# Optimization experiments

Measured on AMD Instinct MI355X. Metric: run time of the kernel, lower is better.

The kernel has to match this reference:

```python
import jax, jax.numpy as jnp
import numpy as np

NUM_HEADS = 12
MASK_BIAS = -1000.0


def setup_inputs() -> dict:
    key = jax.random.key(0)
    k1, k2, k3, k4 = jax.random.split(key, 4)
    B, N, C = 2, 2048, 768
    x = jax.random.normal(k1, (B, N, C), dtype=jnp.float32)
    # key-padding mask: 1.0 = masked-out position (gets -1000 bias), 0.0 = visible
    mask = jax.random.randint(k2, (B, N), 0, 2).astype(jnp.float32)
    qkv_w = jax.random.normal(k3, (3 * C, C), dtype=jnp.float32) * (1.0 / np.sqrt(C))
    proj_w = jax.random.normal(k4, (C, C), dtype=jnp.float32) * (1.0 / np.sqrt(C))
    proj_b = jnp.zeros((C,), dtype=jnp.float32)
    return {"x": x, "mask": mask, "qkv_w": qkv_w, "proj_w": proj_w, "proj_b": proj_b}


def reference(x, mask, qkv_w, proj_w, proj_b):
    B, N, C = x.shape
    H = NUM_HEADS
    D = C // H
    scale = D ** (-0.5)
    # qkv: Linear without bias -> [B, N, 3C] -> [3, B, H, N, D]
    qkv = (x @ qkv_w.T).reshape(B, N, 3, H, D).transpose(2, 0, 3, 1, 4)
    q, k, v = qkv[0], qkv[1], qkv[2]
    # scores [B, H, N, N]
    attn = jnp.einsum("bhqd,bhkd->bhqk", q, k) * scale
    attn = attn + mask[:, None, None, :] * MASK_BIAS
    attn = jax.nn.softmax(attn, axis=-1)
    out = jnp.einsum("bhqk,bhkd->bhqd", attn, v)  # [B, H, N, D]
    out = out.transpose(0, 2, 1, 3).reshape(B, N, C)
    return out @ proj_w.T + proj_b
```

## Files before the change

### kernel.cpp

```cpp
#include <hip/hip_runtime.h>

typedef __bf16 bf16_t;
typedef __bf16 bf16x8 __attribute__((ext_vector_type(8)));
typedef float f32x4 __attribute__((ext_vector_type(4)));

#define NUM_B 2
#define NUM_H 12
#define SEQ_N 2048
#define DIM_C 768
#define HEAD_D 64
#define BH_CNT (NUM_B * NUM_H)
#define MTOK (NUM_B * SEQ_N)
#define QSCALE 0.1803368801111137f

#define AS1(p) ((const __attribute__((address_space(1))) void*)(p))
#define AS3(p) ((__attribute__((address_space(3))) void*)(p))

__global__ __launch_bounds__(256) void cvt_kernel(
    const float* __restrict__ s0, const float* __restrict__ s1,
    const float* __restrict__ s2, const float* __restrict__ msk,
    bf16_t* __restrict__ d0, bf16_t* __restrict__ d1, bf16_t* __restrict__ d2,
    bf16_t* __restrict__ dw, int nb0, int nb1, int nb2) {
  const int blk = blockIdx.x;
  const float* src;
  bf16_t* dst;
  size_t off;
  bool isw = false;
  if (blk < nb0) {
    src = s0; dst = d0; off = (size_t)blk * 2048;
  } else if (blk < nb0 + nb1) {
    src = s1; dst = d1; off = (size_t)(blk - nb0) * 2048;
  } else if (blk < nb0 + nb1 + nb2) {
    src = s2; dst = d2; off = (size_t)(blk - nb0 - nb1) * 2048;
  } else {
    src = msk; dst = dw; off = (size_t)(blk - nb0 - nb1 - nb2) * 2048;
    isw = true;
  }
  const size_t i = off + (size_t)threadIdx.x * 8;
  float4 f0 = *reinterpret_cast<const float4*>(&src[i]);
  float4 f1 = *reinterpret_cast<const float4*>(&src[i + 4]);
  if (isw) {
    f0 = {1.0f - f0.x, 1.0f - f0.y, 1.0f - f0.z, 1.0f - f0.w};
    f1 = {1.0f - f1.x, 1.0f - f1.y, 1.0f - f1.z, 1.0f - f1.w};
  }
  union { ushort4 u; bf16_t h[4]; } p0, p1;
  p0.h[0] = (bf16_t)f0.x; p0.h[1] = (bf16_t)f0.y;
  p0.h[2] = (bf16_t)f0.z; p0.h[3] = (bf16_t)f0.w;
  p1.h[0] = (bf16_t)f1.x; p1.h[1] = (bf16_t)f1.y;
  p1.h[2] = (bf16_t)f1.z; p1.h[3] = (bf16_t)f1.w;
  *reinterpret_cast<ushort4*>(&dst[i]) = p0.u;
  *reinterpret_cast<ushort4*>(&dst[i + 4]) = p1.u;
}

__global__ __launch_bounds__(256, 3) void gemm_qkv_kernel(
    const bf16_t* __restrict__ A, const bf16_t* __restrict__ W,
    const float* __restrict__ mask, bf16_t* __restrict__ out) {
  __shared__ __align__(16) bf16_t As[2][128 * 32];
  __shared__ __align__(16) bf16_t Bs[2][128 * 32];

  const int tid = threadIdx.x;
  const int wave = tid >> 6, lane = tid & 63;
  const int quad = lane >> 4, l16 = lane & 15;
  const int m0 = blockIdx.y * 128, n0 = blockIdx.x * 128;
  const int wm = (wave >> 1) * 64, wn = (wave & 1) * 64;
  const bool vmode = (n0 >= 2 * DIM_C);

  f32x4 acc[4][4] = {};

  const int srow = tid >> 2;
  const int scol = ((tid & 3) ^ ((tid >> 3) & 3)) * 8;
  const bf16_t* gA0 = A + (size_t)(m0 + srow) * DIM_C + scol;
  const bf16_t* gA1 = A + (size_t)(m0 + srow + 64) * DIM_C + scol;
  const bf16_t* gB0 = W + (size_t)(n0 + srow) * DIM_C + scol;
  const bf16_t* gB1 = W + (size_t)(n0 + srow + 64) * DIM_C + scol;
  const int lb = wave * 512;

  auto issue = [&](int buf, int k0) {
    __builtin_amdgcn_global_load_lds(AS1(gA0 + k0), AS3(&As[buf][lb]), 16, 0, 0);
    __builtin_amdgcn_global_load_lds(AS1(gA1 + k0), AS3(&As[buf][lb + 2048]), 16, 0, 0);
    __builtin_amdgcn_global_load_lds(AS1(gB0 + k0), AS3(&Bs[buf][lb]), 16, 0, 0);
    __builtin_amdgcn_global_load_lds(AS1(gB1 + k0), AS3(&Bs[buf][lb + 2048]), 16, 0, 0);
  };

  issue(0, 0);
  int cur = 0;
  const int sw = (l16 >> 1) & 3;
  for (int step = 0; step < DIM_C / 32; ++step) {
    __syncthreads();
    if (step + 1 < DIM_C / 32) issue(cur ^ 1, (step + 1) * 32);

    bf16x8 aF[4], bF[4];
#pragma unroll
    for (int mi = 0; mi < 4; ++mi)
      aF[mi] = *reinterpret_cast<const bf16x8*>(
          &As[cur][(wm + mi * 16 + l16) * 32 + ((quad ^ sw) * 8)]);
#pragma unroll
    for (int ni = 0; ni < 4; ++ni)
      bF[ni] = *reinterpret_cast<const bf16x8*>(
          &Bs[cur][(wn + ni * 16 + l16) * 32 + ((quad ^ sw) * 8)]);
    if (vmode) {
#pragma unroll
      for (int mi = 0; mi < 4; ++mi)
#pragma unroll
        for (int ni = 0; ni < 4; ++ni)
          acc[mi][ni] = __builtin_amdgcn_mfma_f32_16x16x32_bf16(
              bF[ni], aF[mi], acc[mi][ni], 0, 0, 0);
    } else {
#pragma unroll
      for (int mi = 0; mi < 4; ++mi)
#pragma unroll
        for (int ni = 0; ni < 4; ++ni)
          acc[mi][ni] = __builtin_amdgcn_mfma_f32_16x16x32_bf16(
              aF[mi], bF[ni], acc[mi][ni], 0, 0, 0);
    }
    cur ^= 1;
  }

  if (!vmode) {
#pragma unroll
    for (int mi = 0; mi < 4; ++mi) {
#pragma unroll
      for (int ni = 0; ni < 4; ++ni) {
        const int gmB = m0 + wm + mi * 16 + quad * 4;
        const int gn = n0 + wn + ni * 16 + l16;
        const int which = gn / DIM_C;
        const int rem = gn - which * DIM_C;
        const int h = rem >> 6, d = rem & 63;
        const float sc = (which == 0) ? QSCALE : 1.0f;
        const size_t base = (size_t)which * ((size_t)BH_CNT * SEQ_N * HEAD_D);
#pragma unroll
        for (int r = 0; r < 4; ++r) {
          const int gm = gmB + r;
          const int b = gm >> 11, tok = gm & 2047;
          out[base + (((size_t)(b * NUM_H + h) * SEQ_N + tok) * HEAD_D + d)] =
              (bf16_t)(acc[mi][ni][r] * sc);
        }
      }
    }
  } else {
    const size_t base = 2ull * BH_CNT * SEQ_N * HEAD_D;
#pragma unroll
    for (int mi = 0; mi < 4; ++mi) {
      const int tok = m0 + wm + mi * 16 + l16;
      const float wvf = 1.0f - mask[tok];
      const int b = tok >> 11, tokm = tok & 2047;
#pragma unroll
      for (int ni = 0; ni < 4; ++ni) {
#pragma unroll
        for (int r = 0; r < 4; ++r) {
          const int rowg = n0 - 2 * DIM_C + wn + ni * 16 + quad * 4 + r;
          const int h = rowg >> 6, d = rowg & 63;
          out[base + (((size_t)(b * NUM_H + h) * HEAD_D + d) * SEQ_N + tokm)] =
              (bf16_t)(acc[mi][ni][r] * wvf);
        }
      }
    }
  }
}

__global__ __launch_bounds__(256, 4) void gemm_proj_kernel(
    const bf16_t* __restrict__ A, const bf16_t* __restrict__ W,
    const float* __restrict__ bias, float* __restrict__ out) {
  __shared__ __align__(16) bf16_t As[2][64 * 32];
  __shared__ __align__(16) bf16_t Bs[2][64 * 32];

  const int tid = threadIdx.x;
  const int wave = tid >> 6, lane = tid & 63;
  const int quad = lane >> 4, l16 = lane & 15;
  const int m0 = blockIdx.y * 64, n0 = blockIdx.x * 64;
  const int wm = (wave >> 1) * 32, wn = (wave & 1) * 32;

  f32x4 acc[2][2] = {};

  const int srow = tid >> 2;
  const int scol = ((tid & 3) ^ ((tid >> 3) & 3)) * 8;
  const bf16_t* gA = A + (size_t)(m0 + srow) * DIM_C + scol;
  const bf16_t* gB = W + (size_t)(n0 + srow) * DIM_C + scol;
  const int lb = wave * 512;

  auto issue = [&](int buf, int k0) {
    __builtin_amdgcn_global_load_lds(AS1(gA + k0), AS3(&As[buf][lb]), 16, 0, 0);
    __builtin_amdgcn_global_load_lds(AS1(gB + k0), AS3(&Bs[buf][lb]), 16, 0, 0);
  };

  issue(0, 0);
  int cur = 0;
  const int sw = (l16 >> 1) & 3;
  for (int step = 0; step < DIM_C / 32; ++step) {
    __syncthreads();
    if (step + 1 < DIM_C / 32) issue(cur ^ 1, (step + 1) * 32);

    bf16x8 aF[2], bF[2];
#pragma unroll
    for (int mi = 0; mi < 2; ++mi)
      aF[mi] = *reinterpret_cast<const bf16x8*>(
          &As[cur][(wm + mi * 16 + l16) * 32 + ((quad ^ sw) * 8)]);
#pragma unroll
    for (int ni = 0; ni < 2; ++ni)
      bF[ni] = *reinterpret_cast<const bf16x8*>(
          &Bs[cur][(wn + ni * 16 + l16) * 32 + ((quad ^ sw) * 8)]);
#pragma unroll
    for (int mi = 0; mi < 2; ++mi)
#pragma unroll
      for (int ni = 0; ni < 2; ++ni)
        acc[mi][ni] = __builtin_amdgcn_mfma_f32_16x16x32_bf16(aF[mi], bF[ni],
                                                              acc[mi][ni], 0, 0, 0);
    cur ^= 1;
  }

#pragma unroll
  for (int mi = 0; mi < 2; ++mi) {
#pragma unroll
    for (int ni = 0; ni < 2; ++ni) {
      const int gmB = m0 + wm + mi * 16 + quad * 4;
      const int gn = n0 + wn + ni * 16 + l16;
      const float bv = bias[gn];
#pragma unroll
      for (int r = 0; r < 4; ++r)
        out[(size_t)(gmB + r) * DIM_C + gn] = acc[mi][ni][r] + bv;
    }
  }
}

__global__ __launch_bounds__(256, 4) void attn_kernel(
    const bf16_t* __restrict__ q, const bf16_t* __restrict__ k,
    const bf16_t* __restrict__ vt, const bf16_t* __restrict__ wv,
    bf16_t* __restrict__ ctx) {
  __shared__ __align__(16) bf16_t Ks[2][64 * 64];
  __shared__ __align__(16) bf16_t Vs[2][64 * 64];
  __shared__ __align__(16) bf16_t Ps[4][1024];

  const int tid = threadIdx.x;
  const int wave = tid >> 6, lane = tid & 63;
  const int quad = lane >> 4, l16 = lane & 15;
  const int bh = blockIdx.y;
  const int b = bh / NUM_H, h = bh - b * NUM_H;
  const int q0 = blockIdx.x * 64 + wave * 16;

  const bf16_t* qb = q + (size_t)bh * SEQ_N * HEAD_D;
  const bf16_t* kb = k + (size_t)bh * SEQ_N * HEAD_D;
  const bf16_t* vtb = vt + (size_t)bh * HEAD_D * SEQ_N;
  const bf16_t* wb = wv + (size_t)b * SEQ_N;

  bf16x8 qf[2];
#pragma unroll
  for (int ks = 0; ks < 2; ++ks)
    qf[ks] = *reinterpret_cast<const bf16x8*>(
        &qb[(size_t)(q0 + l16) * HEAD_D + ks * 32 + quad * 8]);

  f32x4 acc[4] = {};
  f32x4 acc_l = {};

  const int srow = tid >> 3;
  const int scol = ((tid & 7) ^ ((tid >> 3) & 7)) * 8;
  const bf16_t* gK0 = kb + (size_t)srow * HEAD_D + scol;
  const bf16_t* gK1 = kb + (size_t)(srow + 32) * HEAD_D + scol;
  const bf16_t* gV0 = vtb + (size_t)srow * SEQ_N + scol;
  const bf16_t* gV1 = vtb + (size_t)(srow + 32) * SEQ_N + scol;
  const int lb = wave * 512;

  auto issueKV = [&](int buf, int key0) {
    __builtin_amdgcn_global_load_lds(AS1(gK0 + (size_t)key0 * HEAD_D),
                                     AS3(&Ks[buf][lb]), 16, 0, 0);
    __builtin_amdgcn_global_load_lds(AS1(gK1 + (size_t)key0 * HEAD_D),
                                     AS3(&Ks[buf][lb + 2048]), 16, 0, 0);
    __builtin_amdgcn_global_load_lds(AS1(gV0 + key0), AS3(&Vs[buf][lb]), 16, 0, 0);
    __builtin_amdgcn_global_load_lds(AS1(gV1 + key0), AS3(&Vs[buf][lb + 2048]),
                                     16, 0, 0);
  };

  issueKV(0, 0);
  int cur = 0;
  const int swz = l16 & 7;
  const int psbase = wave * 1024 + l16 * 64;
  for (int key0 = 0; key0 < SEQ_N; key0 += 64) {
    __syncthreads();
    if (key0 + 64 < SEQ_N) issueKV(cur ^ 1, key0 + 64);

    f32x4 s[4];
#pragma unroll
    for (int kt = 0; kt < 4; ++kt) {
      const int row = kt * 16 + l16;
      bf16x8 kf0 = *reinterpret_cast<const bf16x8*>(
          &Ks[cur][row * 64 + ((quad ^ swz) * 8)]);
      bf16x8 kf1 = *reinterpret_cast<const bf16x8*>(
          &Ks[cur][row * 64 + (((4 + quad) ^ swz) * 8)]);
      f32x4 z = {0.0f, 0.0f, 0.0f, 0.0f};
      z = __builtin_amdgcn_mfma_f32_16x16x32_bf16(kf0, qf[0], z, 0, 0, 0);
      s[kt] = __builtin_amdgcn_mfma_f32_16x16x32_bf16(kf1, qf[1], z, 0, 0, 0);
    }

#pragma unroll
    for (int kt = 0; kt < 4; ++kt) {
      union { ushort4 u; bf16_t h4[4]; } pk;
      pk.h4[0] = (bf16_t)exp2f(s[kt][0]);
      pk.h4[1] = (bf16_t)exp2f(s[kt][1]);
      pk.h4[2] = (bf16_t)exp2f(s[kt][2]);
      pk.h4[3] = (bf16_t)exp2f(s[kt][3]);
      const int c = kt * 2 + (quad >> 1);
      *reinterpret_cast<ushort4*>(
          &Ps[0][psbase + ((c ^ swz) << 3) + ((quad & 1) << 2)]) = pk.u;
    }

    bf16x8 pf0 = *reinterpret_cast<const bf16x8*>(
        &Ps[0][psbase + ((quad ^ swz) << 3)]);
    bf16x8 pf1 = *reinterpret_cast<const bf16x8*>(
        &Ps[0][psbase + (((4 + quad) ^ swz) << 3)]);
    bf16x8 wf0 = *reinterpret_cast<const bf16x8*>(&wb[key0 + quad * 8]);
    bf16x8 wf1 = *reinterpret_cast<const bf16x8*>(&wb[key0 + 32 + quad * 8]);
    acc_l = __builtin_amdgcn_mfma_f32_16x16x32_bf16(pf0, wf0, acc_l, 0, 0, 0);
    acc_l = __builtin_amdgcn_mfma_f32_16x16x32_bf16(pf1, wf1, acc_l, 0, 0, 0);

#pragma unroll
    for (int dt = 0; dt < 4; ++dt) {
      const int row = dt * 16 + l16;
      bf16x8 vf0 = *reinterpret_cast<const bf16x8*>(
          &Vs[cur][row * 64 + ((quad ^ swz) * 8)]);
      bf16x8 vf1 = *reinterpret_cast<const bf16x8*>(
          &Vs[cur][row * 64 + (((4 + quad) ^ swz) * 8)]);
      acc[dt] = __builtin_amdgcn_mfma_f32_16x16x32_bf16(pf0, vf0, acc[dt], 0, 0, 0);
      acc[dt] = __builtin_amdgcn_mfma_f32_16x16x32_bf16(pf1, vf1, acc[dt], 0, 0, 0);
    }
    cur ^= 1;
  }

  float rl[4];
#pragma unroll
  for (int r = 0; r < 4; ++r) rl[r] = 1.0f / acc_l[r];
#pragma unroll
  for (int dt = 0; dt < 4; ++dt)
#pragma unroll
    for (int r = 0; r < 4; ++r) {
      const int tok = q0 + quad * 4 + r;
      ctx[((size_t)b * SEQ_N + tok) * DIM_C + h * HEAD_D + dt * 16 + l16] =
          (bf16_t)(acc[dt][r] * rl[r]);
    }
}

extern "C" void kernel_launch(void* const* d_in, const int* in_sizes, int n_in,
                              void* d_out, int out_size, void* d_ws,
                              size_t ws_size, hipStream_t stream) {
  const float* x = (const float*)d_in[0];
  const float* mask = (const float*)d_in[1];
  const float* qkv_w = (const float*)d_in[2];
  const float* proj_w = (const float*)d_in[3];
  const float* proj_b = (const float*)d_in[4];
  float* out = (float*)d_out;

  const size_t nx = (size_t)MTOK * DIM_C;
  const size_t nqw = (size_t)3 * DIM_C * DIM_C;
  const size_t npw = (size_t)DIM_C * DIM_C;
  const size_t nmask = (size_t)NUM_B * SEQ_N;
  const size_t per = (size_t)BH_CNT * SEQ_N * HEAD_D;

  bf16_t* xb = (bf16_t*)d_ws;
  bf16_t* qwb = xb + nx;
  bf16_t* pwb = qwb + nqw;
  bf16_t* wvb = pwb + npw;
  bf16_t* qkv = wvb + nmask;
  bf16_t* ctx = qkv + 3 * per;

  const int nb0 = (int)(nx / 2048), nb1 = (int)(nqw / 2048),
            nb2 = (int)(npw / 2048), nbm = (int)(nmask / 2048);

  cvt_kernel<<<nb0 + nb1 + nb2 + nbm, 256, 0, stream>>>(
      x, qkv_w, proj_w, mask, xb, qwb, pwb, wvb, nb0, nb1, nb2);
  gemm_qkv_kernel<<<dim3(3 * DIM_C / 128, MTOK / 128), 256, 0, stream>>>(
      xb, qwb, mask, qkv);
  attn_kernel<<<dim3(SEQ_N / 64, BH_CNT), 256, 0, stream>>>(
      qkv, qkv + per, qkv + 2 * per, wvb, ctx);
  gemm_proj_kernel<<<dim3(DIM_C / 64, MTOK / 64), 256, 0, stream>>>(
      ctx, pwb, proj_b, out);
}
```

Before: 175.0 us.

## Compact visible keys via mask scan and skip masked keys in attention

```diff
diff --git a/kernel.cpp b/kernel.cpp
--- a/kernel.cpp
+++ b/kernel.cpp
@@ -16,45 +16,80 @@
 #define AS1(p) ((const __attribute__((address_space(1))) void*)(p))
 #define AS3(p) ((__attribute__((address_space(3))) void*)(p))
 
-__global__ __launch_bounds__(256) void cvt_kernel(
+__global__ __launch_bounds__(256) void cvt_scan_kernel(
     const float* __restrict__ s0, const float* __restrict__ s1,
     const float* __restrict__ s2, const float* __restrict__ msk,
     bf16_t* __restrict__ d0, bf16_t* __restrict__ d1, bf16_t* __restrict__ d2,
-    bf16_t* __restrict__ dw, int nb0, int nb1, int nb2) {
+    int* __restrict__ src, bf16_t* __restrict__ wp, int* __restrict__ cnts,
+    int nb0, int nb1, int nb2) {
+  __shared__ int psum[256];
   const int blk = blockIdx.x;
-  const float* src;
-  bf16_t* dst;
+  const int t = threadIdx.x;
+  if (blk >= nb0 + nb1 + nb2) {
+    const int b = blk - (nb0 + nb1 + nb2);
+    const float* mb = msk + (size_t)b * SEQ_N;
+    int vis[8], c = 0;
+#pragma unroll
+    for (int j = 0; j < 8; ++j) {
+      vis[j] = (mb[t * 8 + j] == 0.0f) ? 1 : 0;
+      c += vis[j];
+    }
+    psum[t] = c;
+    __syncthreads();
+    for (int off = 1; off < 256; off <<= 1) {
+      int v = (t >= off) ? psum[t - off] : 0;
+      __syncthreads();
+      psum[t] += v;
+      __syncthreads();
+    }
+    const int total = psum[255];
+    int vpos = psum[t] - c;
+    int mpos = total + (t * 8 - (psum[t] - c));
+#pragma unroll
+    for (int j = 0; j < 8; ++j) {
+      const int tok = t * 8 + j;
+      if (vis[j]) {
+        src[b * SEQ_N + vpos] = b * SEQ_N + tok;
+        wp[b * SEQ_N + vpos] = (bf16_t)1.0f;
+        ++vpos;
+      } else {
+        src[b * SEQ_N + mpos] = b * SEQ_N + tok;
+        wp[b * SEQ_N + mpos] = (bf16_t)0.0f;
+        ++mpos;
+      }
+    }
+    if (t == 0) {
+      cnts[b * 2] = (total + 63) & ~63;
+      cnts[b * 2 + 1] = total;
+    }
+    return;
+  }
+  const float* sp;
+  bf16_t* dp;
   size_t off;
-  bool isw = false;
   if (blk < nb0) {
-    src = s0; dst = d0; off = (size_t)blk * 2048;
+    sp = s0; dp = d0; off = (size_t)blk * 2048;
   } else if (blk < nb0 + nb1) {
-    src = s1; dst = d1; off = (size_t)(blk - nb0) * 2048;
-  } else if (blk < nb0 + nb1 + nb2) {
-    src = s2; dst = d2; off = (size_t)(blk - nb0 - nb1) * 2048;
+    sp = s1; dp = d1; off = (size_t)(blk - nb0) * 2048;
   } else {
-    src = msk; dst = dw; off = (size_t)(blk - nb0 - nb1 - nb2) * 2048;
-    isw = true;
-  }
-  const size_t i = off + (size_t)threadIdx.x * 8;
-  float4 f0 = *reinterpret_cast<const float4*>(&src[i]);
-  float4 f1 = *reinterpret_cast<const float4*>(&src[i + 4]);
-  if (isw) {
-    f0 = {1.0f - f0.x, 1.0f - f0.y, 1.0f - f0.z, 1.0f - f0.w};
-    f1 = {1.0f - f1.x, 1.0f - f1.y, 1.0f - f1.z, 1.0f - f1.w};
-  }
+    sp = s2; dp = d2; off = (size_t)(blk - nb0 - nb1) * 2048;
+  }
+  const size_t i = off + (size_t)t * 8;
+  float4 f0 = *reinterpret_cast<const float4*>(&sp[i]);
+  float4 f1 = *reinterpret_cast<const float4*>(&sp[i + 4]);
   union { ushort4 u; bf16_t h[4]; } p0, p1;
   p0.h[0] = (bf16_t)f0.x; p0.h[1] = (bf16_t)f0.y;
   p0.h[2] = (bf16_t)f0.z; p0.h[3] = (bf16_t)f0.w;
   p1.h[0] = (bf16_t)f1.x; p1.h[1] = (bf16_t)f1.y;
   p1.h[2] = (bf16_t)f1.z; p1.h[3] = (bf16_t)f1.w;
-  *reinterpret_cast<ushort4*>(&dst[i]) = p0.u;
-  *reinterpret_cast<ushort4*>(&dst[i + 4]) = p1.u;
+  *reinterpret_cast<ushort4*>(&dp[i]) = p0.u;
+  *reinterpret_cast<ushort4*>(&dp[i + 4]) = p1.u;
 }
 
 __global__ __launch_bounds__(256, 3) void gemm_qkv_kernel(
     const bf16_t* __restrict__ A, const bf16_t* __restrict__ W,
-    const float* __restrict__ mask, bf16_t* __restrict__ out) {
+    const int* __restrict__ src, const int* __restrict__ cnts,
+    bf16_t* __restrict__ out) {
   __shared__ __align__(16) bf16_t As[2][128 * 32];
   __shared__ __align__(16) bf16_t Bs[2][128 * 32];
 
@@ -63,7 +98,117 @@
   const int quad = lane >> 4, l16 = lane & 15;
   const int m0 = blockIdx.y * 128, n0 = blockIdx.x * 128;
   const int wm = (wave >> 1) * 64, wn = (wave & 1) * 64;
-  const bool vmode = (n0 >= 2 * DIM_C);
+  const bool isQ = (n0 < DIM_C);
+
+  if (!isQ) {
+    const int b = m0 >> 11;
+    if ((m0 & 2047) >= cnts[b * 2]) return;
+  }
+
+  f32x4 acc[4][4] = {};
+
+  const int srow = tid >> 2;
+  const int scol = ((tid & 3) ^ ((tid >> 3) & 3)) * 8;
+  int ar0, ar1;
+  if (isQ) {
+    ar0 = m0 + srow;
+    ar1 = m0 + srow + 64;
+  } else {
+    ar0 = src[m0 + srow];
+    ar1 = src[m0 + srow + 64];
+  }
+  const bf16_t* gA0 = A + (size_t)ar0 * DIM_C + scol;
+  const bf16_t* gA1 = A + (size_t)ar1 * DIM_C + scol;
+  const bf16_t* gB0 = W + (size_t)(n0 + srow) * DIM_C + scol;
+  const bf16_t* gB1 = W + (size_t)(n0 + srow + 64) * DIM_C + scol;
+  const int lb = wave * 512;
+
+  auto issue = [&](int buf, int k0) {
+    __builtin_amdgcn_global_load_lds(AS1(gA0 + k0), AS3(&As[buf][lb]), 16, 0, 0);
+    __builtin_amdgcn_global_load_lds(AS1(gA1 + k0), AS3(&As[buf][lb + 2048]), 16, 0, 0);
+    __builtin_amdgcn_global_load_lds(AS1(gB0 + k0), AS3(&Bs[buf][lb]), 16, 0, 0);
+    __builtin_amdgcn_global_load_lds(AS1(gB1 + k0), AS3(&Bs[buf][lb + 2048]), 16, 0, 0);
+  };
+
+  issue(0, 0);
+  int cur = 0;
+  const int sw = (l16 >> 1) & 3;
+  for (int step = 0; step < DIM_C / 32; ++step) {
+    __syncthreads();
+    if (step + 1 < DIM_C / 32) issue(cur ^ 1, (step + 1) * 32);
+
+    bf16x8 aF[4], bF[4];
+#pragma unroll
+    for (int mi = 0; mi < 4; ++mi)
+      aF[mi] = *reinterpret_cast<const bf16x8*>(
+          &As[cur][(wm + mi * 16 + l16) * 32 + ((quad ^ sw) * 8)]);
+#pragma unroll
+    for (int ni = 0; ni < 4; ++ni)
+      bF[ni] = *reinterpret_cast<const bf16x8*>(
+          &Bs[cur][(wn + ni * 16 + l16) * 32 + ((quad ^ sw) * 8)]);
+#pragma unroll
+    for (int mi = 0; mi < 4; ++mi)
+#pragma unroll
+      for (int ni = 0; ni < 4; ++ni)
+        acc[mi][ni] = __builtin_amdgcn_mfma_f32_16x16x32_bf16(aF[mi], bF[ni],
+                                                              acc[mi][ni], 0, 0, 0);
+    cur ^= 1;
+  }
+
+  const size_t per = (size_t)BH_CNT * SEQ_N * HEAD_D;
+#pragma unroll
+  for (int mi = 0; mi < 4; ++mi) {
+#pragma unroll
+    for (int ni = 0; ni < 4; ++ni) {
+      const int gmB = m0 + wm + mi * 16 + quad * 4;
+      const int gn = n0 + wn + ni * 16 + l16;
+      const int b = gmB >> 11;
+      if (isQ) {
+        const int h = gn >> 6, d = gn & 63;
+#pragma unroll
+        for (int r = 0; r < 4; ++r) {
+          const int gm = gmB + r;
+          const int tok = gm & 2047;
+          out[(((size_t)((gm >> 11) * NUM_H + h) * SEQ_N + tok) * HEAD_D + d)] =
+              (bf16_t)(acc[mi][ni][r] * QSCALE);
+        }
+      } else if (n0 < 2 * DIM_C) {
+        const int rem = gn - DIM_C;
+        const int h = rem >> 6, d = rem & 63;
+#pragma unroll
+        for (int r = 0; r < 4; ++r) {
+          const int pos = (gmB + r) & 2047;
+          out[per + (((size_t)(b * NUM_H + h) * SEQ_N + pos) * HEAD_D + d)] =
+              (bf16_t)acc[mi][ni][r];
+        }
+      } else {
+        const int rem = gn - 2 * DIM_C;
+        const int h = rem >> 6, d = rem & 63;
+        const int pos0 = gmB & 2047;
+        const int count = cnts[b * 2 + 1];
+        union { ushort4 u; bf16_t h4[4]; } pk;
+#pragma unroll
+        for (int r = 0; r < 4; ++r)
+          pk.h4[r] = (pos0 + r < count) ? (bf16_t)acc[mi][ni][r] : (bf16_t)0.0f;
+        *reinterpret_cast<ushort4*>(
+            &out[2 * per + (((size_t)(b * NUM_H + h) * HEAD_D + d) * SEQ_N + pos0)]) =
+            pk.u;
+      }
+    }
+  }
+}
+
+__global__ __launch_bounds__(256, 3) void gemm_proj_kernel(
+    const bf16_t* __restrict__ A, const bf16_t* __restrict__ W,
+    const float* __restrict__ bias, float* __restrict__ out) {
+  __shared__ __align__(16) bf16_t As[2][128 * 32];
+  __shared__ __align__(16) bf16_t Bs[2][128 * 32];
+
+  const int tid = threadIdx.x;
+  const int wave = tid >> 6, lane = tid & 63;
+  const int quad = lane >> 4, l16 = lane & 15;
+  const int m0 = blockIdx.y * 128, n0 = blockIdx.x * 128;
+  const int wm = (wave >> 1) * 64, wn = (wave & 1) * 64;
 
   f32x4 acc[4][4] = {};
 
@@ -98,120 +243,19 @@
     for (int ni = 0; ni < 4; ++ni)
       bF[ni] = *reinterpret_cast<const bf16x8*>(
           &Bs[cur][(wn + ni * 16 + l16) * 32 + ((quad ^ sw) * 8)]);
-    if (vmode) {
-#pragma unroll
-      for (int mi = 0; mi < 4; ++mi)
-#pragma unroll
-        for (int ni = 0; ni < 4; ++ni)
-          acc[mi][ni] = __builtin_amdgcn_mfma_f32_16x16x32_bf16(
-              bF[ni], aF[mi], acc[mi][ni], 0, 0, 0);
-    } else {
-#pragma unroll
-      for (int mi = 0; mi < 4; ++mi)
-#pragma unroll
-        for (int ni = 0; ni < 4; ++ni)
-          acc[mi][ni] = __builtin_amdgcn_mfma_f32_16x16x32_bf16(
-              aF[mi], bF[ni], acc[mi][ni], 0, 0, 0);
-    }
-    cur ^= 1;
-  }
-
-  if (!vmode) {
-#pragma unroll
-    for (int mi = 0; mi < 4; ++mi) {
-#pragma unroll
-      for (int ni = 0; ni < 4; ++ni) {
-        const int gmB = m0 + wm + mi * 16 + quad * 4;
-        const int gn = n0 + wn + ni * 16 + l16;
-        const int which = gn / DIM_C;
-        const int rem = gn - which * DIM_C;
-        const int h = rem >> 6, d = rem & 63;
-        const float sc = (which == 0) ? QSCALE : 1.0f;
-        const size_t base = (size_t)which * ((size_t)BH_CNT * SEQ_N * HEAD_D);
-#pragma unroll
-        for (int r = 0; r < 4; ++r) {
-          const int gm = gmB + r;
-          const int b = gm >> 11, tok = gm & 2047;
-          out[base + (((size_t)(b * NUM_H + h) * SEQ_N + tok) * HEAD_D + d)] =
-              (bf16_t)(acc[mi][ni][r] * sc);
-        }
-      }
-    }
-  } else {
-    const size_t base = 2ull * BH_CNT * SEQ_N * HEAD_D;
-#pragma unroll
-    for (int mi = 0; mi < 4; ++mi) {
-      const int tok = m0 + wm + mi * 16 + l16;
-      const float wvf = 1.0f - mask[tok];
-      const int b = tok >> 11, tokm = tok & 2047;
-#pragma unroll
-      for (int ni = 0; ni < 4; ++ni) {
-#pragma unroll
-        for (int r = 0; r < 4; ++r) {
-          const int rowg = n0 - 2 * DIM_C + wn + ni * 16 + quad * 4 + r;
-          const int h = rowg >> 6, d = rowg & 63;
-          out[base + (((size_t)(b * NUM_H + h) * HEAD_D + d) * SEQ_N + tokm)] =
-              (bf16_t)(acc[mi][ni][r] * wvf);
-        }
-      }
-    }
-  }
-}
-
-__global__ __launch_bounds__(256, 4) void gemm_proj_kernel(
-    const bf16_t* __restrict__ A, const bf16_t* __restrict__ W,
-    const float* __restrict__ bias, float* __restrict__ out) {
-  __shared__ __align__(16) bf16_t As[2][64 * 32];
-  __shared__ __align__(16) bf16_t Bs[2][64 * 32];
-
-  const int tid = threadIdx.x;
-  const int wave = tid >> 6, lane = tid & 63;
-  const int quad = lane >> 4, l16 = lane & 15;
-  const int m0 = blockIdx.y * 64, n0 = blockIdx.x * 64;
-  const int wm = (wave >> 1) * 32, wn = (wave & 1) * 32;
-
-  f32x4 acc[2][2] = {};
-
-  const int srow = tid >> 2;
-  const int scol = ((tid & 3) ^ ((tid >> 3) & 3)) * 8;
-  const bf16_t* gA = A + (size_t)(m0 + srow) * DIM_C + scol;
-  const bf16_t* gB = W + (size_t)(n0 + srow) * DIM_C + scol;
-  const int lb = wave * 512;
-
-  auto issue = [&](int buf, int k0) {
-    __builtin_amdgcn_global_load_lds(AS1(gA + k0), AS3(&As[buf][lb]), 16, 0, 0);
-    __builtin_amdgcn_global_load_lds(AS1(gB + k0), AS3(&Bs[buf][lb]), 16, 0, 0);
-  };
-
-  issue(0, 0);
-  int cur = 0;
-  const int sw = (l16 >> 1) & 3;
-  for (int step = 0; step < DIM_C / 32; ++step) {
-    __syncthreads();
-    if (step + 1 < DIM_C / 32) issue(cur ^ 1, (step + 1) * 32);
-
-    bf16x8 aF[2], bF[2];
-#pragma unroll
-    for (int mi = 0; mi < 2; ++mi)
-      aF[mi] = *reinterpret_cast<const bf16x8*>(
-          &As[cur][(wm + mi * 16 + l16) * 32 + ((quad ^ sw) * 8)]);
-#pragma unroll
-    for (int ni = 0; ni < 2; ++ni)
-      bF[ni] = *reinterpret_cast<const bf16x8*>(
-          &Bs[cur][(wn + ni * 16 + l16) * 32 + ((quad ^ sw) * 8)]);
-#pragma unroll
-    for (int mi = 0; mi < 2; ++mi)
-#pragma unroll
-      for (int ni = 0; ni < 2; ++ni)
+#pragma unroll
+    for (int mi = 0; mi < 4; ++mi)
+#pragma unroll
+      for (int ni = 0; ni < 4; ++ni)
         acc[mi][ni] = __builtin_amdgcn_mfma_f32_16x16x32_bf16(aF[mi], bF[ni],
                                                               acc[mi][ni], 0, 0, 0);
     cur ^= 1;
   }
 
 #pragma unroll
-  for (int mi = 0; mi < 2; ++mi) {
-#pragma unroll
-    for (int ni = 0; ni < 2; ++ni) {
+  for (int mi = 0; mi < 4; ++mi) {
+#pragma unroll
+    for (int ni = 0; ni < 4; ++ni) {
       const int gmB = m0 + wm + mi * 16 + quad * 4;
       const int gn = n0 + wn + ni * 16 + l16;
       const float bv = bias[gn];
@@ -224,8 +268,8 @@
 
 __global__ __launch_bounds__(256, 4) void attn_kernel(
     const bf16_t* __restrict__ q, const bf16_t* __restrict__ k,
-    const bf16_t* __restrict__ vt, const bf16_t* __restrict__ wv,
-    bf16_t* __restrict__ ctx) {
+    const bf16_t* __restrict__ vt, const bf16_t* __restrict__ wp,
+    const int* __restrict__ cnts, bf16_t* __restrict__ ctx) {
   __shared__ __align__(16) bf16_t Ks[2][64 * 64];
   __shared__ __align__(16) bf16_t Vs[2][64 * 64];
   __shared__ __align__(16) bf16_t Ps[4][1024];
@@ -236,11 +280,12 @@
   const int bh = blockIdx.y;
   const int b = bh / NUM_H, h = bh - b * NUM_H;
   const int q0 = blockIdx.x * 64 + wave * 16;
+  const int cntPad = cnts[b * 2];
 
   const bf16_t* qb = q + (size_t)bh * SEQ_N * HEAD_D;
   const bf16_t* kb = k + (size_t)bh * SEQ_N * HEAD_D;
   const bf16_t* vtb = vt + (size_t)bh * HEAD_D * SEQ_N;
-  const bf16_t* wb = wv + (size_t)b * SEQ_N;
+  const bf16_t* wb = wp + (size_t)b * SEQ_N;
 
   bf16x8 qf[2];
 #pragma unroll
@@ -273,9 +318,9 @@
   int cur = 0;
   const int swz = l16 & 7;
   const int psbase = wave * 1024 + l16 * 64;
-  for (int key0 = 0; key0 < SEQ_N; key0 += 64) {
+  for (int key0 = 0; key0 < cntPad; key0 += 64) {
     __syncthreads();
-    if (key0 + 64 < SEQ_N) issueKV(cur ^ 1, key0 + 64);
+    if (key0 + 64 < cntPad) issueKV(cur ^ 1, key0 + 64);
 
     f32x4 s[4];
 #pragma unroll
@@ -350,25 +395,26 @@
   const size_t nx = (size_t)MTOK * DIM_C;
   const size_t nqw = (size_t)3 * DIM_C * DIM_C;
   const size_t npw = (size_t)DIM_C * DIM_C;
-  const size_t nmask = (size_t)NUM_B * SEQ_N;
   const size_t per = (size_t)BH_CNT * SEQ_N * HEAD_D;
 
   bf16_t* xb = (bf16_t*)d_ws;
   bf16_t* qwb = xb + nx;
   bf16_t* pwb = qwb + nqw;
-  bf16_t* wvb = pwb + npw;
-  bf16_t* qkv = wvb + nmask;
+  bf16_t* wpb = pwb + npw;
+  int* srcb = (int*)(wpb + MTOK);
+  int* cntsb = srcb + MTOK;
+  bf16_t* qkv = (bf16_t*)(cntsb + 8);
   bf16_t* ctx = qkv + 3 * per;
 
   const int nb0 = (int)(nx / 2048), nb1 = (int)(nqw / 2048),
-            nb2 = (int)(npw / 2048), nbm = (int)(nmask / 2048);
-
-  cvt_kernel<<<nb0 + nb1 + nb2 + nbm, 256, 0, stream>>>(
-      x, qkv_w, proj_w, mask, xb, qwb, pwb, wvb, nb0, nb1, nb2);
+            nb2 = (int)(npw / 2048);
+
+  cvt_scan_kernel<<<nb0 + nb1 + nb2 + NUM_B, 256, 0, stream>>>(
+      x, qkv_w, proj_w, mask, xb, qwb, pwb, srcb, wpb, cntsb, nb0, nb1, nb2);
   gemm_qkv_kernel<<<dim3(3 * DIM_C / 128, MTOK / 128), 256, 0, stream>>>(
-      xb, qwb, mask, qkv);
+      xb, qwb, srcb, cntsb, qkv);
   attn_kernel<<<dim3(SEQ_N / 64, BH_CNT), 256, 0, stream>>>(
-      qkv, qkv + per, qkv + 2 * per, wvb, ctx);
-  gemm_proj_kernel<<<dim3(DIM_C / 64, MTOK / 64), 256, 0, stream>>>(
+      qkv, qkv + per, qkv + 2 * per, wpb, cntsb, ctx);
+  gemm_proj_kernel<<<dim3(DIM_C / 128, MTOK / 128), 256, 0, stream>>>(
       ctx, pwb, proj_b, out);
 }
```

Result: faster. 150.5 us (-14.0%).
